# Kernel tuning notes

Measured on AMD Instinct MI355X. Metric: run time of the kernel, lower is better.

## Reference

```python
import jax, jax.numpy as jnp
import numpy as np

G = 3  # group_num
EPS = 1e-5


def _ln(x, g, b):
    m = x.mean(-1, keepdims=True)
    v = x.var(-1, keepdims=True)
    return (x - m) / jnp.sqrt(v + EPS) * g + b


def _gcm(x, w_qk, b_qk, ct_w1, ct_b1, ct_g, ct_be, ct_w2, ct_b2,
         lw_w1, lw_b1, lw_g, lw_be, lw_w2, lw_b2):
    # x: [B, 768, H, W] (pre-concatenated group feature)
    b, c, h, w = x.shape
    gc = c // G
    # channel shuffle: b (g c) h w -> b (c g) h w
    xs = x.reshape(b, G, gc, h, w).transpose(0, 2, 1, 3, 4).reshape(b, c, h, w)
    out = xs.reshape(b, G, gc, h, w)            # b g c h w
    value = out.reshape(b, G, gc, h * w)        # b g c n
    # fc_qk (Linear gc->1) over the channel axis, softmax over spatial n
    logits = jnp.einsum('bgcn,c->bgn', value, w_qk) + b_qk
    attn = jax.nn.softmax(logits, axis=-1)       # b g n
    context = jnp.einsum('bgcn,bgn->bgc', value, attn)  # b g c
    lvl_context = context.reshape(b, c)          # b (g c)
    # ctx_transform: Linear -> LN -> ReLU -> Linear
    h1 = jax.nn.relu(_ln(context @ ct_w1.T + ct_b1, ct_g, ct_be))
    ctx = h1 @ ct_w2.T + ct_b2                   # b g c
    # lvl_weight: Linear -> LN -> ReLU -> Linear -> Sigmoid
    l1 = jax.nn.relu(_ln(lvl_context @ lw_w1.T + lw_b1, lw_g, lw_be))
    lvlw = jax.nn.sigmoid(l1 @ lw_w2.T + lw_b2)  # b g (=3)
    ctx = ctx * lvlw[:, :, None]
    return (out + ctx[:, :, :, None, None]).sum(axis=1)  # b c_g h w


def setup_inputs() -> dict:
    key = jax.random.key(0)
    ks = jax.random.split(key, 16)
    B = 8
    sizes = [(128, 128), (64, 64), (32, 32), (16, 16)]
    inp = {}
    for i, (h, w) in enumerate(sizes):
        inp[f'g{i}'] = jax.random.normal(ks[i], (B, 768, h, w), jnp.float32)
    inp['x_last'] = jax.random.normal(ks[4], (B, 256, 8, 8), jnp.float32)
    s = 0.05
    inp['w_qk'] = jax.random.normal(ks[5], (4, 256), jnp.float32) * s
    inp['b_qk'] = jax.random.normal(ks[6], (4,), jnp.float32) * s
    inp['ct_w1'] = jax.random.normal(ks[7], (4, 64, 256), jnp.float32) * s
    inp['ct_b1'] = jax.random.normal(ks[8], (4, 64), jnp.float32) * s
    inp['ct_g'] = jnp.ones((4, 64), jnp.float32)
    inp['ct_be'] = jnp.zeros((4, 64), jnp.float32)
    inp['ct_w2'] = jax.random.normal(ks[9], (4, 256, 64), jnp.float32) * s
    inp['ct_b2'] = jax.random.normal(ks[10], (4, 256), jnp.float32) * s
    inp['lw_w1'] = jax.random.normal(ks[11], (4, 768, 768), jnp.float32) * s
    inp['lw_b1'] = jax.random.normal(ks[12], (4, 768), jnp.float32) * s
    inp['lw_g'] = jnp.ones((4, 768), jnp.float32)
    inp['lw_be'] = jnp.zeros((4, 768), jnp.float32)
    inp['lw_w2'] = jax.random.normal(ks[13], (4, 3, 768), jnp.float32) * s
    inp['lw_b2'] = jax.random.normal(ks[14], (4, 3), jnp.float32) * s
    return inp


def reference(g0, g1, g2, g3, x_last, w_qk, b_qk, ct_w1, ct_b1, ct_g, ct_be,
              ct_w2, ct_b2, lw_w1, lw_b1, lw_g, lw_be, lw_w2, lw_b2):
    outs = []
    for i, g in enumerate([g0, g1, g2, g3]):
        outs.append(_gcm(g, w_qk[i], b_qk[i], ct_w1[i], ct_b1[i], ct_g[i],
                         ct_be[i], ct_w2[i], ct_b2[i], lw_w1[i], lw_b1[i],
                         lw_g[i], lw_be[i], lw_w2[i], lw_b2[i]))
    return (*outs, x_last)
```

## Files before the change

### kernel.cpp

```cpp
#include <hip/hip_runtime.h>

#define NB 8
#define NTILE 5440
#define PSTRIDE 772

typedef float f4 __attribute__((ext_vector_type(4)));

__device__ __forceinline__ f4 ntload(const float* p) {
  return __builtin_nontemporal_load((const f4*)p);
}
__device__ __forceinline__ void ntstore(float* p, f4 v) {
  __builtin_nontemporal_store(v, (f4*)p);
}
__device__ __forceinline__ float hsum(f4 v) { return v.x + v.y + v.z + v.w; }

struct KFArgs {
  const float* x[4];
  float* outp[4];
  float* partial;
  int N[4];
};

__global__ __launch_bounds__(512, 4) void kf_fused(KFArgs a, const float* __restrict__ wqk_all) {
  __shared__ float red[768];
  __shared__ float zl[24];

  int wg = blockIdx.x;
  int lvl, b, idx;
  if (wg < 4096)      { lvl = 0; b = wg >> 9;            idx = wg & 511; }
  else if (wg < 5120) { int r = wg - 4096; lvl = 1; b = r >> 7; idx = r & 127; }
  else if (wg < 5376) { int r = wg - 5120; lvl = 2; b = r >> 5; idx = r & 31; }
  else                { int r = wg - 5376; lvl = 3; b = r >> 3; idx = r & 7; }
  int N = a.N[lvl];
  const float* __restrict__ xb = a.x[lvl] + (size_t)b * 768 * N;
  float* __restrict__ outb = a.outp[lvl] + (size_t)b * 256 * N;
  int tid = threadIdx.x;
  int snq = tid & 7, oq = tid >> 3, wv = tid >> 6;
  int n0 = idx * 32 + snq * 4;

  int srow[4][3];
  float wq[4];
#pragma unroll
  for (int j = 0; j < 4; ++j) {
    int c2 = oq + 64 * j;
    wq[j] = wqk_all[lvl * 256 + c2];
#pragma unroll
    for (int k = 0; k < 3; ++k) {
      int f = c2 + (k << 8);
      srow[j][k] = (f % 3) * 256 + f / 3;
    }
  }

  f4 X[12];
#pragma unroll
  for (int j = 0; j < 4; ++j)
#pragma unroll
    for (int k = 0; k < 3; ++k)
      X[j * 3 + k] = ntload(xb + (size_t)srow[j][k] * N + n0);

  f4 pg[3] = {{0.f, 0.f, 0.f, 0.f}, {0.f, 0.f, 0.f, 0.f}, {0.f, 0.f, 0.f, 0.f}};
#pragma unroll
  for (int j = 0; j < 4; ++j)
#pragma unroll
    for (int k = 0; k < 3; ++k)
      pg[k] += X[j * 3 + k] * wq[j];
#pragma unroll
  for (int k = 0; k < 3; ++k) {
#pragma unroll
    for (int m = 8; m <= 32; m <<= 1) {
      pg[k].x += __shfl_xor(pg[k].x, m);
      pg[k].y += __shfl_xor(pg[k].y, m);
      pg[k].z += __shfl_xor(pg[k].z, m);
      pg[k].w += __shfl_xor(pg[k].w, m);
    }
  }
  if ((tid & 63) < 8) {
#pragma unroll
    for (int k = 0; k < 3; ++k)
      *(f4*)(red + (wv * 24 + k * 8 + snq) * 4) = pg[k];
  }
  asm volatile("s_waitcnt lgkmcnt(0)" ::: "memory");
  __builtin_amdgcn_sched_barrier(0);
  __builtin_amdgcn_s_barrier();
  __builtin_amdgcn_sched_barrier(0);

  f4 sev[3];
#pragma unroll
  for (int k = 0; k < 3; ++k) {
    f4 s = {0.f, 0.f, 0.f, 0.f};
#pragma unroll
    for (int w = 0; w < 8; ++w) s += *(const f4*)(red + (w * 24 + k * 8 + snq) * 4);
    f4 e;
    e.x = __expf(s.x); e.y = __expf(s.y); e.z = __expf(s.z); e.w = __expf(s.w);
    sev[k] = e;
  }
  if (tid < 8) {
#pragma unroll
    for (int k = 0; k < 3; ++k) zl[tid * 3 + k] = hsum(sev[k]);
  }

  float acc[4][3];
#pragma unroll
  for (int j = 0; j < 4; ++j) {
    f4 ov = X[j * 3 + 0] + X[j * 3 + 1] + X[j * 3 + 2];
    *(f4*)(outb + (size_t)(oq + 64 * j) * N + n0) = ov;
#pragma unroll
    for (int k = 0; k < 3; ++k)
      acc[j][k] = hsum(X[j * 3 + k] * sev[k]);
  }

  float* pw = a.partial + (size_t)wg * PSTRIDE;
#pragma unroll
  for (int j = 0; j < 4; ++j)
#pragma unroll
    for (int k = 0; k < 3; ++k) {
      float v = acc[j][k];
      v += __shfl_xor(v, 1);
      v += __shfl_xor(v, 2);
      v += __shfl_xor(v, 4);
      if (snq == 0) pw[k * 256 + oq + 64 * j] = v;
    }
  __syncthreads();
  if (tid < 3) {
    float z = 0.f;
#pragma unroll
    for (int s = 0; s < 8; ++s) z += zl[s * 3 + tid];
    pw[768 + tid] = z;
  }
}

__device__ __forceinline__ float blk_sum256(float v, float* sr4) {
  for (int o = 32; o; o >>= 1) v += __shfl_xor(v, o);
  __syncthreads();
  if ((threadIdx.x & 63) == 0) sr4[threadIdx.x >> 6] = v;
  __syncthreads();
  return sr4[0] + sr4[1] + sr4[2] + sr4[3];
}

__global__ __launch_bounds__(256) void k4_mlp(
    const float* __restrict__ partial,
    const float* __restrict__ ct_w1, const float* __restrict__ ct_b1,
    const float* __restrict__ ct_g,  const float* __restrict__ ct_be,
    const float* __restrict__ ct_w2, const float* __restrict__ ct_b2,
    const float* __restrict__ lw_w1, const float* __restrict__ lw_b1,
    const float* __restrict__ lw_g,  const float* __restrict__ lw_be,
    const float* __restrict__ lw_w2, const float* __restrict__ lw_b2,
    float* __restrict__ add_all) {
  int b = blockIdx.x, lvl = blockIdx.y;
  int t = threadIdx.x;
  static const int cnt_[4] = {512, 128, 32, 8};
  static const int base_[4] = {0, 4096, 5120, 5376};
  int cnt = cnt_[lvl];
  int wg0 = base_[lvl] + b * cnt;

  const float* w1 = ct_w1 + lvl * 64 * 256;
  const float* b1 = ct_b1 + lvl * 64;
  const float* cg = ct_g + lvl * 64;
  const float* cbe = ct_be + lvl * 64;
  const float* w2 = ct_w2 + lvl * 256 * 64;
  const float* b2 = ct_b2 + lvl * 256;
  const float* W1 = lw_w1 + (size_t)lvl * 768 * 768;
  const float* B1 = lw_b1 + lvl * 768;
  const float* Lg = lw_g + lvl * 768;
  const float* Lbe = lw_be + lvl * 768;
  const float* W2 = lw_w2 + lvl * 3 * 768;
  const float* B2 = lw_b2 + lvl * 3;
  float* addp = add_all + ((size_t)lvl * NB + b) * 256;

  __shared__ float sctx[768];
  __shared__ float sh1[3][64];
  __shared__ float sl1[768];
  __shared__ float slvlw[3];
  __shared__ float sr4[4];
  __shared__ float sZ[3];
  __shared__ float zp[96];

  if (t < 96) {
    int g = t >> 5, j = t & 31;
    float z = 0.f;
    for (int w = j; w < cnt; w += 32)
      z += partial[(size_t)(wg0 + w) * PSTRIDE + 768 + g];
    zp[t] = z;
  }
  float s0 = 0.f, s1 = 0.f, s2 = 0.f;
#pragma unroll 8
  for (int w = 0; w < cnt; ++w) {
    const float* pw = partial + (size_t)(wg0 + w) * PSTRIDE;
    s0 += pw[t];
    s1 += pw[t + 256];
    s2 += pw[t + 512];
  }
  __syncthreads();
  if (t < 3) {
    float z = 0.f;
#pragma unroll
    for (int i = 0; i < 32; ++i) z += zp[t * 32 + i];
    sZ[t] = z;
  }
  __syncthreads();
  sctx[t] = s0 / sZ[0];
  sctx[t + 256] = s1 / sZ[1];
  sctx[t + 512] = s2 / sZ[2];
  __syncthreads();

  if (t < 192) {
    int g = t >> 6, j = t & 63;
    const f4* w4 = (const f4*)(w1 + j * 256);
    const f4* c4 = (const f4*)(sctx + g * 256);
    f4 acc = {0.f, 0.f, 0.f, 0.f};
#pragma unroll 8
    for (int k = 0; k < 64; ++k) acc += c4[k] * w4[k];
    sh1[g][j] = hsum(acc) + b1[j];
  }
  __syncthreads();
  int wv = t >> 6, ln = t & 63;
  if (wv < 3) {
    float v = sh1[wv][ln];
    float s = v;
    for (int o = 32; o; o >>= 1) s += __shfl_xor(s, o);
    float mean = s * (1.f / 64.f);
    float d = v - mean;
    float q = d * d;
    for (int o = 32; o; o >>= 1) q += __shfl_xor(q, o);
    float var = q * (1.f / 64.f);
    float y = d * rsqrtf(var + 1e-5f) * cg[ln] + cbe[ln];
    sh1[wv][ln] = fmaxf(y, 0.f);
  }
  __syncthreads();
  float l1v[3];
#pragma unroll
  for (int r = 0; r < 3; ++r) {
    int j = t + r * 256;
    const f4* W4 = (const f4*)(W1 + (size_t)j * 768);
    const f4* s4 = (const f4*)sctx;
    f4 acc = {0.f, 0.f, 0.f, 0.f};
#pragma unroll 8
    for (int k = 0; k < 192; ++k) acc += s4[k] * W4[k];
    l1v[r] = hsum(acc) + B1[j];
  }
  float S = blk_sum256(l1v[0] + l1v[1] + l1v[2], sr4);
  float mean = S * (1.f / 768.f);
  float q = 0.f;
#pragma unroll
  for (int r = 0; r < 3; ++r) { float d = l1v[r] - mean; q += d * d; }
  float var = blk_sum256(q, sr4) * (1.f / 768.f);
  float inv = rsqrtf(var + 1e-5f);
#pragma unroll
  for (int r = 0; r < 3; ++r) {
    int j = t + r * 256;
    float y = (l1v[r] - mean) * inv * Lg[j] + Lbe[j];
    sl1[j] = fmaxf(y, 0.f);
  }
  __syncthreads();
  if (wv < 3) {
    float acc = 0.f;
    for (int j = ln; j < 768; j += 64) acc = fmaf(sl1[j], W2[wv * 768 + j], acc);
    for (int o = 32; o; o >>= 1) acc += __shfl_xor(acc, o);
    if (ln == 0) slvlw[wv] = 1.f / (1.f + __expf(-(acc + B2[wv])));
  }
  __syncthreads();
  {
    int c2 = t;
    float a = 0.f;
#pragma unroll
    for (int g = 0; g < 3; ++g) {
      const f4* w4 = (const f4*)(w2 + c2 * 64);
      const f4* h4 = (const f4*)(sh1[g]);
      f4 acc = {0.f, 0.f, 0.f, 0.f};
#pragma unroll
      for (int j = 0; j < 16; ++j) acc += h4[j] * w4[j];
      a += (hsum(acc) + b2[c2]) * slvlw[g];
    }
    addp[c2] = a;
  }
}

__global__ __launch_bounds__(256) void k5_add(float* __restrict__ out,
                                              const float* __restrict__ add_all,
                                              const float* __restrict__ xlast) {
  size_t f4i = (size_t)blockIdx.x * 256 + threadIdx.x;
  if (f4i >= 11141120) {
    size_t r = f4i - 11141120;
    f4 v = ntload(xlast + (r << 2));
    ntstore(out + (f4i << 2), v);
    return;
  }
  int lvl, lgN2;
  size_t base;
  if (f4i < 8388608)       { lvl = 0; base = 0;        lgN2 = 12; }
  else if (f4i < 10485760) { lvl = 1; base = 8388608;  lgN2 = 10; }
  else if (f4i < 11010048) { lvl = 2; base = 10485760; lgN2 = 8;  }
  else                     { lvl = 3; base = 11010048; lgN2 = 6;  }
  size_t lf4 = f4i - base;
  int bc = (int)(lf4 >> lgN2);
  float a = add_all[lvl * 2048 + bc];
  float* p = out + (f4i << 2);
  f4 v = *(const f4*)p;
  v += a;
  ntstore(p, v);
}

extern "C" void kernel_launch(void* const* d_in, const int* in_sizes, int n_in,
                              void* d_out, int out_size, void* d_ws, size_t ws_size,
                              hipStream_t stream) {
  const float* gx[4] = {(const float*)d_in[0], (const float*)d_in[1],
                        (const float*)d_in[2], (const float*)d_in[3]};
  const float* x_last = (const float*)d_in[4];
  const float* w_qk = (const float*)d_in[5];
  const float* ct_w1 = (const float*)d_in[7];
  const float* ct_b1 = (const float*)d_in[8];
  const float* ct_g  = (const float*)d_in[9];
  const float* ct_be = (const float*)d_in[10];
  const float* ct_w2 = (const float*)d_in[11];
  const float* ct_b2 = (const float*)d_in[12];
  const float* lw_w1 = (const float*)d_in[13];
  const float* lw_b1 = (const float*)d_in[14];
  const float* lw_g  = (const float*)d_in[15];
  const float* lw_be = (const float*)d_in[16];
  const float* lw_w2 = (const float*)d_in[17];
  const float* lw_b2 = (const float*)d_in[18];
  float* out = (float*)d_out;
  float* ws = (float*)d_ws;

  static const int Ns[4] = {16384, 4096, 1024, 256};
  static const size_t outOff[4] = {0, 33554432, 41943040, 44040192};

  float* partb = ws;
  float* addb  = ws + (size_t)NTILE * PSTRIDE;

  KFArgs af;
  for (int i = 0; i < 4; ++i) {
    af.x[i] = gx[i];
    af.outp[i] = out + outOff[i];
    af.N[i] = Ns[i];
  }
  af.partial = partb;

  kf_fused<<<dim3(NTILE), dim3(512), 0, stream>>>(af, w_qk);
  k4_mlp<<<dim3(NB, 4), dim3(256), 0, stream>>>(partb, ct_w1, ct_b1, ct_g, ct_be,
                                                ct_w2, ct_b2, lw_w1, lw_b1, lw_g,
                                                lw_be, lw_w2, lw_b2, addb);
  k5_add<<<dim3(43648), dim3(256), 0, stream>>>(out, addb, x_last);
}
```

Measured before the change: 316.2 us.

## Widen fused pass tiles to 128 spatial positions per workgroup

Each workgroup of the fused pass now covers 128 spatial positions instead of 32, with each thread holding 16x3 vector loads. This cuts the workgroup count and the number of per-tile partial records (768 context sums plus 3 softmax denominators) by a factor of four, which shrinks the partial buffer the MLP kernel must reduce. The denominator reduction is rewritten with shuffles in place of a separate shared array and barrier. In exchange each thread needs far more registers (launch bounds drop to one block per CU hint), occupancy falls, and the per-channel shuffle reductions grow from three to five steps.

```diff
diff --git a/kernel.cpp b/kernel.cpp
--- a/kernel.cpp
+++ b/kernel.cpp
@@ -1,7 +1,7 @@
 #include <hip/hip_runtime.h>
 
 #define NB 8
-#define NTILE 5440
+#define NTILE 1360
 #define PSTRIDE 772
 
 typedef float f4 __attribute__((ext_vector_type(4)));
@@ -21,111 +21,97 @@
   int N[4];
 };
 
-__global__ __launch_bounds__(512, 4) void kf_fused(KFArgs a, const float* __restrict__ wqk_all) {
-  __shared__ float red[768];
-  __shared__ float zl[24];
+__global__ __launch_bounds__(512, 1) void kf_fused(KFArgs a, const float* __restrict__ wqk_all) {
+  __shared__ float red[8 * 3 * 32 * 4];
 
   int wg = blockIdx.x;
   int lvl, b, idx;
-  if (wg < 4096)      { lvl = 0; b = wg >> 9;            idx = wg & 511; }
-  else if (wg < 5120) { int r = wg - 4096; lvl = 1; b = r >> 7; idx = r & 127; }
-  else if (wg < 5376) { int r = wg - 5120; lvl = 2; b = r >> 5; idx = r & 31; }
-  else                { int r = wg - 5376; lvl = 3; b = r >> 3; idx = r & 7; }
+  if (wg < 1024)      { lvl = 0; b = wg >> 7;            idx = wg & 127; }
+  else if (wg < 1280) { int r = wg - 1024; lvl = 1; b = r >> 5; idx = r & 31; }
+  else if (wg < 1344) { int r = wg - 1280; lvl = 2; b = r >> 3; idx = r & 7; }
+  else                { int r = wg - 1344; lvl = 3; b = r >> 1; idx = r & 1; }
   int N = a.N[lvl];
   const float* __restrict__ xb = a.x[lvl] + (size_t)b * 768 * N;
   float* __restrict__ outb = a.outp[lvl] + (size_t)b * 256 * N;
   int tid = threadIdx.x;
-  int snq = tid & 7, oq = tid >> 3, wv = tid >> 6;
-  int n0 = idx * 32 + snq * 4;
-
-  int srow[4][3];
-  float wq[4];
-#pragma unroll
-  for (int j = 0; j < 4; ++j) {
-    int c2 = oq + 64 * j;
-    wq[j] = wqk_all[lvl * 256 + c2];
+  int snq = tid & 31, oq = tid >> 5, wv = tid >> 6;
+  int n0 = idx * 128 + snq * 4;
+
+  float wq[16];
+  const float* __restrict__ wqk = wqk_all + lvl * 256;
+#pragma unroll
+  for (int j = 0; j < 16; ++j) wq[j] = wqk[oq + 16 * j];
+
+  f4 X[16][3];
+#pragma unroll
+  for (int j = 0; j < 16; ++j)
 #pragma unroll
     for (int k = 0; k < 3; ++k) {
-      int f = c2 + (k << 8);
-      srow[j][k] = (f % 3) * 256 + f / 3;
+      int f = oq + 16 * j + 256 * k;
+      int row = (f % 3) * 256 + f / 3;
+      X[j][k] = ntload(xb + (size_t)row * N + n0);
     }
-  }
-
-  f4 X[12];
-#pragma unroll
-  for (int j = 0; j < 4; ++j)
+
+  f4 pg[3] = {{0.f, 0.f, 0.f, 0.f}, {0.f, 0.f, 0.f, 0.f}, {0.f, 0.f, 0.f, 0.f}};
+#pragma unroll
+  for (int j = 0; j < 16; ++j)
 #pragma unroll
     for (int k = 0; k < 3; ++k)
-      X[j * 3 + k] = ntload(xb + (size_t)srow[j][k] * N + n0);
-
-  f4 pg[3] = {{0.f, 0.f, 0.f, 0.f}, {0.f, 0.f, 0.f, 0.f}, {0.f, 0.f, 0.f, 0.f}};
-#pragma unroll
-  for (int j = 0; j < 4; ++j)
+      pg[k] += X[j][k] * wq[j];
+#pragma unroll
+  for (int k = 0; k < 3; ++k) {
+    pg[k].x += __shfl_xor(pg[k].x, 32);
+    pg[k].y += __shfl_xor(pg[k].y, 32);
+    pg[k].z += __shfl_xor(pg[k].z, 32);
+    pg[k].w += __shfl_xor(pg[k].w, 32);
+  }
+  if ((tid & 32) == 0) {
 #pragma unroll
     for (int k = 0; k < 3; ++k)
-      pg[k] += X[j * 3 + k] * wq[j];
-#pragma unroll
-  for (int k = 0; k < 3; ++k) {
-#pragma unroll
-    for (int m = 8; m <= 32; m <<= 1) {
-      pg[k].x += __shfl_xor(pg[k].x, m);
-      pg[k].y += __shfl_xor(pg[k].y, m);
-      pg[k].z += __shfl_xor(pg[k].z, m);
-      pg[k].w += __shfl_xor(pg[k].w, m);
-    }
-  }
-  if ((tid & 63) < 8) {
-#pragma unroll
-    for (int k = 0; k < 3; ++k)
-      *(f4*)(red + (wv * 24 + k * 8 + snq) * 4) = pg[k];
-  }
-  asm volatile("s_waitcnt lgkmcnt(0)" ::: "memory");
-  __builtin_amdgcn_sched_barrier(0);
-  __builtin_amdgcn_s_barrier();
-  __builtin_amdgcn_sched_barrier(0);
+      *(f4*)(red + ((wv * 3 + k) * 32 + snq) * 4) = pg[k];
+  }
+  __syncthreads();
 
   f4 sev[3];
 #pragma unroll
   for (int k = 0; k < 3; ++k) {
     f4 s = {0.f, 0.f, 0.f, 0.f};
 #pragma unroll
-    for (int w = 0; w < 8; ++w) s += *(const f4*)(red + (w * 24 + k * 8 + snq) * 4);
+    for (int w = 0; w < 8; ++w) s += *(const f4*)(red + ((w * 3 + k) * 32 + snq) * 4);
     f4 e;
     e.x = __expf(s.x); e.y = __expf(s.y); e.z = __expf(s.z); e.w = __expf(s.w);
     sev[k] = e;
   }
-  if (tid < 8) {
-#pragma unroll
-    for (int k = 0; k < 3; ++k) zl[tid * 3 + k] = hsum(sev[k]);
-  }
-
-  float acc[4][3];
-#pragma unroll
-  for (int j = 0; j < 4; ++j) {
-    f4 ov = X[j * 3 + 0] + X[j * 3 + 1] + X[j * 3 + 2];
-    *(f4*)(outb + (size_t)(oq + 64 * j) * N + n0) = ov;
-#pragma unroll
-    for (int k = 0; k < 3; ++k)
-      acc[j][k] = hsum(X[j * 3 + k] * sev[k]);
-  }
 
   float* pw = a.partial + (size_t)wg * PSTRIDE;
-#pragma unroll
-  for (int j = 0; j < 4; ++j)
+  if (tid < 32) {
 #pragma unroll
     for (int k = 0; k < 3; ++k) {
-      float v = acc[j][k];
+      float z = hsum(sev[k]);
+      z += __shfl_xor(z, 1);
+      z += __shfl_xor(z, 2);
+      z += __shfl_xor(z, 4);
+      z += __shfl_xor(z, 8);
+      z += __shfl_xor(z, 16);
+      if (tid == 0) pw[768 + k] = z;
+    }
+  }
+
+#pragma unroll
+  for (int j = 0; j < 16; ++j) {
+    int c2 = oq + 16 * j;
+    f4 ov = X[j][0] + X[j][1] + X[j][2];
+    *(f4*)(outb + (size_t)c2 * N + n0) = ov;
+#pragma unroll
+    for (int k = 0; k < 3; ++k) {
+      float v = hsum(X[j][k] * sev[k]);
       v += __shfl_xor(v, 1);
       v += __shfl_xor(v, 2);
       v += __shfl_xor(v, 4);
-      if (snq == 0) pw[k * 256 + oq + 64 * j] = v;
+      v += __shfl_xor(v, 8);
+      v += __shfl_xor(v, 16);
+      if (snq == 0) pw[k * 256 + c2] = v;
     }
-  __syncthreads();
-  if (tid < 3) {
-    float z = 0.f;
-#pragma unroll
-    for (int s = 0; s < 8; ++s) z += zl[s * 3 + tid];
-    pw[768 + tid] = z;
   }
 }
 
@@ -148,8 +134,8 @@
     float* __restrict__ add_all) {
   int b = blockIdx.x, lvl = blockIdx.y;
   int t = threadIdx.x;
-  static const int cnt_[4] = {512, 128, 32, 8};
-  static const int base_[4] = {0, 4096, 5120, 5376};
+  static const int cnt_[4] = {128, 32, 8, 2};
+  static const int base_[4] = {0, 1024, 1280, 1344};
   int cnt = cnt_[lvl];
   int wg0 = base_[lvl] + b * cnt;
 
```

Result: faster. 303.5 us (-4.0%).
